# Kernel optimization log

Measured on AMD Instinct MI355X. Metric: run time of the kernel, lower is better.

Reference implementation:

```python
import jax, jax.numpy as jnp
import numpy as np
import math

N_HEAD = 16
N_EMBD = 2048
HEAD_DIM = 128
N_LAYER = 24
EPS = 1e-5


def _get_alibi_slopes(n_heads):
    def pow2(n):
        start = 2 ** (-2 ** (-(math.log2(n) - 3)))
        return [start * start ** i for i in range(n)]
    if math.log2(n_heads).is_integer():
        return pow2(n_heads)
    c = 2 ** math.floor(math.log2(n_heads))
    s = pow2(c)
    extra = _get_alibi_slopes(2 * c)
    return s + extra[0::2][: n_heads - c]

ALIBI_SLOPES = jnp.asarray(np.array(_get_alibi_slopes(N_HEAD), dtype=np.float32))  # (H,)


def rmsnorm(x, w, eps=EPS):
    # fp32 RMSNorm over last dim with affine weight (use_fp32=True path)
    xf = x.astype(jnp.float32)
    out = xf * jax.lax.rsqrt(jnp.mean(xf * xf, axis=-1, keepdims=True) + eps)
    return (out * w.astype(jnp.float32)).astype(x.dtype)


def setup_inputs() -> dict:
    key = jax.random.key(0)
    ks = jax.random.split(key, 8)
    B, T, C, H, D = 2, 2048, N_EMBD, N_HEAD, HEAD_DIM
    sc = 1.0 / math.sqrt(C)
    proj_std = 0.5 / math.sqrt(C) / math.sqrt(N_LAYER)
    return {
        "x": jax.random.normal(ks[0], (B, T, C), jnp.float32),
        "Wq": jax.random.normal(ks[1], (C, H * D), jnp.float32) * sc,
        "Wk": jax.random.normal(ks[2], (C, H * D), jnp.float32) * sc,
        "Wv": jax.random.normal(ks[3], (C, H * D), jnp.float32) * sc,
        "Wproj": jax.random.normal(ks[4], (H * D, C), jnp.float32) * proj_std,
        "q_rms_w": jnp.ones((D,), jnp.float32),
        "k_rms_w": jnp.ones((D,), jnp.float32),
        "subln_w": jnp.ones((D,), jnp.float32),
    }


def reference(x, Wq, Wk, Wv, Wproj, q_rms_w, k_rms_w, subln_w):
    B, T, C = x.shape
    H, D = N_HEAD, HEAD_DIM
    q = (x @ Wq).reshape(B, T, H, D)
    k = (x @ Wk).reshape(B, T, H, D)
    v = (x @ Wv).reshape(B, T, H, D)
    # QK RMSNorm over head_dim
    q = rmsnorm(q, q_rms_w)
    k = rmsnorm(k, k_rms_w)
    # ALiBi bias: -slope * max(i-j, 0), plus causal mask
    idx = jnp.arange(T)
    dist = jnp.maximum(idx[:, None] - idx[None, :], 0).astype(jnp.float32)  # (T,T)
    bias = -dist[None, :, :] * ALIBI_SLOPES[:, None, None]  # (H,T,T)
    causal = idx[:, None] >= idx[None, :]  # (T,T)
    scale = 1.0 / math.sqrt(D)
    scores = jnp.einsum("bthd,bshd->bhts", q, k) * scale + bias[None]  # (B,H,T,T)
    scores = jnp.where(causal[None, None], scores, -jnp.inf)
    attn = jax.nn.softmax(scores, axis=-1)
    y = jnp.einsum("bhts,bshd->bhtd", attn, v)  # (B,H,T,D)
    y = rmsnorm(y, subln_w)  # post-attention groupnorm (subln)
    y = y.transpose(0, 2, 1, 3).reshape(B, T, H * D)
    return y @ Wproj
```

## Files before the change

### kernel.cpp

```cpp
#include <hip/hip_runtime.h>
#include <hip/hip_bf16.h>

#define Bc 2
#define Tc 2048
#define Cc 2048
#define Hc 16
#define Dc 128
#define BTc 4096
#define NQ 6144
#define EPSc 1e-5f
#define QSCALE 0.08838834764831845f

typedef __attribute__((ext_vector_type(8))) short bf16x8;
typedef __attribute__((ext_vector_type(4))) short bf16x4;
typedef __attribute__((ext_vector_type(4))) float f32x4;

typedef struct { unsigned short u[4]; } us4;

__device__ __forceinline__ f32x4 mfma16(bf16x8 a, bf16x8 b, f32x4 c) {
  return __builtin_amdgcn_mfma_f32_16x16x32_bf16(a, b, c, 0, 0, 0);
}

__device__ __forceinline__ void gload16(const void* g, void* l) {
  __builtin_amdgcn_global_load_lds(
      (const __attribute__((address_space(1))) void*)g,
      (__attribute__((address_space(3))) void*)l, 16, 0, 0);
}

__global__ __launch_bounds__(256) void k_xconv(const float* __restrict__ x,
                                               __hip_bfloat16* __restrict__ xb) {
  size_t i = ((size_t)blockIdx.x * 256 + threadIdx.x) * 4;
  float4 v = *(const float4*)(x + i);
  union { __hip_bfloat16 h[4]; bf16x4 v4; } u;
  u.h[0] = __float2bfloat16(v.x); u.h[1] = __float2bfloat16(v.y);
  u.h[2] = __float2bfloat16(v.z); u.h[3] = __float2bfloat16(v.w);
  *(bf16x4*)(xb + i) = u.v4;
}

__global__ __launch_bounds__(256) void k_wconv(const float* __restrict__ Wq,
    const float* __restrict__ Wk, const float* __restrict__ Wv,
    const float* __restrict__ Wp, __hip_bfloat16* __restrict__ Wqkv_t,
    __hip_bfloat16* __restrict__ Wproj_t) {
  __shared__ float tile[64][65];
  int z = blockIdx.z;
  const float* src = (z == 0) ? Wq : (z == 1) ? Wk : (z == 2) ? Wv : Wp;
  __hip_bfloat16* dst = (z < 3) ? (Wqkv_t + (size_t)z * Cc * Cc) : Wproj_t;
  int k0 = blockIdx.x * 64, n0 = blockIdx.y * 64;
  int c = threadIdx.x & 63, rb = threadIdx.x >> 6;
  for (int i = 0; i < 16; i++) {
    int r = rb * 16 + i;
    tile[r][c] = src[(size_t)(k0 + r) * Cc + n0 + c];
  }
  __syncthreads();
  for (int i = 0; i < 16; i++) {
    int r = rb * 16 + i;
    dst[(size_t)(n0 + r) * Cc + k0 + c] = __float2bfloat16(tile[c][r]);
  }
}

__device__ __forceinline__ void mm48(f32x4 (&acc)[4][8], const bf16x8 (&A_)[4],
                                     const bf16x8 (&B_)[8]) {
  __builtin_amdgcn_s_setprio(1);
#pragma unroll
  for (int m = 0; m < 4; m++)
#pragma unroll
    for (int n = 0; n < 8; n++)
      acc[m][n] = mfma16(A_[m], B_[n], acc[m][n]);
  __builtin_amdgcn_s_setprio(0);
}

template <int MODE, typename OutT>
__global__ __launch_bounds__(256, 2) void k_gemm4(const __hip_bfloat16* __restrict__ A,
    const __hip_bfloat16* __restrict__ Bt, OutT* __restrict__ Co,
    int M, int N, const float* __restrict__ qw, const float* __restrict__ kw,
    __hip_bfloat16* __restrict__ Vt) {
  constexpr int K = 2048;
  __shared__ __align__(16) char lds[73728];
  const int nbx = M >> 7;
  const int nwg = nbx * (N >> 8);
  const int wg = blockIdx.x;
  const int swz = (wg & 7) * (nwg >> 3) + (wg >> 3);
  const int bx = swz % nbx, by = swz / nbx;
  const int tid = threadIdx.x, lane = tid & 63, wid = tid >> 6;
  const int wr = wid >> 1, wc = wid & 1;
  const int lr = lane & 15, lg = lane >> 4;
  const int xs = lg ^ ((lr >> 1) & 3);
  const int aoffR = (wr * 64 + lr) * 64 + xs * 16;
  const int boffR = 8192 + (wc * 128 + lr) * 64 + xs * 16;
  const int srow = lane >> 2;
  const int scolE = (((lane & 3) ^ ((lane >> 3) & 3)) << 3);
  const __hip_bfloat16* Ag = A + (size_t)(bx * 128 + wid * 32 + srow) * K + scolE;
  const __hip_bfloat16* Bg = Bt + (size_t)(by * 256 + wid * 64 + srow) * K + scolE;
  const size_t rK16 = (size_t)16 * K;
  char* dA = lds + wid * 2048;
  char* dB = lds + 8192 + wid * 4096;

#define STG(BUF, TS) {                                                   \
    gload16(Ag + (TS) * 32,        dA + (BUF) * 24576);                  \
    gload16(Ag + rK16 + (TS) * 32, dA + (BUF) * 24576 + 1024);           \
    gload16(Bg + (TS) * 32,            dB + (BUF) * 24576);              \
    gload16(Bg + rK16 + (TS) * 32,     dB + (BUF) * 24576 + 1024);       \
    gload16(Bg + 2 * rK16 + (TS) * 32, dB + (BUF) * 24576 + 2048);       \
    gload16(Bg + 3 * rK16 + (TS) * 32, dB + (BUF) * 24576 + 3072);       \
  }
#define BARRIER asm volatile("s_barrier" ::: "memory")
#define VW6 asm volatile("s_waitcnt vmcnt(6)" ::: "memory")
#define VW0 asm volatile("s_waitcnt vmcnt(0)" ::: "memory")

  f32x4 acc[4][8];
#pragma unroll
  for (int m = 0; m < 4; m++)
#pragma unroll
    for (int n = 0; n < 8; n++) acc[m][n] = f32x4{0.f, 0.f, 0.f, 0.f};
  bf16x8 rA[4], rB[8];

#define PH(RB, SB, TS, DOSTG, ENDW) {                                    \
    _Pragma("unroll")                                                    \
    for (int m = 0; m < 4; m++)                                          \
      rA[m] = *(const bf16x8*)(lds + (RB) * 24576 + aoffR + m * 1024);   \
    _Pragma("unroll")                                                    \
    for (int n = 0; n < 8; n++)                                          \
      rB[n] = *(const bf16x8*)(lds + (RB) * 24576 + boffR + n * 1024);   \
    if (DOSTG) STG((SB), (TS));                                          \
    mm48(acc, rA, rB);                                                   \
    ENDW;                                                                \
    BARRIER;                                                             \
  }

  STG(0, 0); STG(1, 1);
  VW6;
  BARRIER;

  for (int i = 0; i < 20; ++i) {
    const int t = 3 * i;
    PH(0, 2, t + 2, 1, VW6);
    PH(1, 0, t + 3, 1, VW6);
    PH(2, 1, t + 4, 1, VW6);
  }
  PH(0, 2, 62, 1, VW6);
  PH(1, 0, 63, 1, VW6);
  PH(2, 0, 0, 0, VW0);
  PH(0, 0, 0, 0, (void)0);
#undef PH
#undef STG
#undef BARRIER
#undef VW6
#undef VW0

  const int row0 = bx * 128 + wr * 64 + lg * 4;
  const int col0 = by * 256 + wc * 128 + lr;

  if (MODE == 1) {
    const int region = by >> 3;
    if (region < 2) {
      const float* wsel = (region == 0) ? qw : kw;
      const float extra = (region == 0) ? QSCALE : 1.0f;
      float wv[8];
#pragma unroll
      for (int n = 0; n < 8; n++) wv[n] = wsel[n * 16 + lr];
#pragma unroll
      for (int m = 0; m < 4; m++) {
        float ss[4] = {0.f, 0.f, 0.f, 0.f};
#pragma unroll
        for (int n = 0; n < 8; n++)
#pragma unroll
          for (int r = 0; r < 4; r++) ss[r] += acc[m][n][r] * acc[m][n][r];
        for (int msk = 1; msk < 16; msk <<= 1)
#pragma unroll
          for (int r = 0; r < 4; r++) ss[r] += __shfl_xor(ss[r], msk);
        float sc[4];
#pragma unroll
        for (int r = 0; r < 4; r++)
          sc[r] = rsqrtf(ss[r] * (1.0f / Dc) + EPSc) * extra;
#pragma unroll
        for (int n = 0; n < 8; n++) {
          size_t base = (size_t)(row0 + m * 16) * N + col0 + n * 16;
#pragma unroll
          for (int r = 0; r < 4; r++)
            ((__hip_bfloat16*)Co)[base + (size_t)r * N] =
                __float2bfloat16(acc[m][n][r] * sc[r] * wv[n]);
        }
      }
    } else {
      const int h = ((by - 16) * 256 + wc * 128) >> 7;
      const int bat = bx >> 4;
#pragma unroll
      for (int m = 0; m < 4; m++) {
        const int t0 = (row0 + m * 16) & (Tc - 1);
#pragma unroll
        for (int n = 0; n < 8; n++) {
          union { us4 p; unsigned long long q; } u;
#pragma unroll
          for (int r = 0; r < 4; r++) {
            union { __hip_bfloat16 h16; unsigned short s; } cv;
            cv.h16 = __float2bfloat16(acc[m][n][r]);
            u.p.u[r] = cv.s;
          }
          __hip_bfloat16* dst = Vt +
              ((size_t)(bat * 16 + h) * 128 + n * 16 + lr) * Tc + t0;
          *(unsigned long long*)dst = u.q;
        }
      }
    }
  } else {
#pragma unroll
    for (int m = 0; m < 4; m++)
#pragma unroll
      for (int n = 0; n < 8; n++) {
        size_t base = (size_t)(row0 + m * 16) * N + col0 + n * 16;
#pragma unroll
        for (int r = 0; r < 4; r++) {
          float v = acc[m][n][r];
          if constexpr (sizeof(OutT) == 2)
            Co[base + (size_t)r * N] = __float2bfloat16(v);
          else
            Co[base + (size_t)r * N] = v;
        }
      }
  }
}

__global__ __launch_bounds__(256, 2) void k_attn(const __hip_bfloat16* __restrict__ QKV,
    const __hip_bfloat16* __restrict__ Vt, const float* __restrict__ subw,
    __hip_bfloat16* __restrict__ Y) {
  __shared__ __align__(16) __hip_bfloat16 Ks[2][64][128];
  __shared__ __align__(16) __hip_bfloat16 Vs[2][128][64];
  __shared__ __align__(16) __hip_bfloat16 Plds[4][16][72];
  const int bh = blockIdx.x, pp = blockIdx.y;
  const int b = bh >> 4, h = bh & 15;
  const int w = threadIdx.x >> 6, lane = threadIdx.x & 63;
  const int lr = lane & 15, lg = lane >> 4;
  const float slope = exp2f(-0.5f * (float)(h + 1));
  const __hip_bfloat16* Kbase = QKV + (size_t)b * Tc * NQ + Cc + h * Dc;
  const __hip_bfloat16* Vbase = Vt + (size_t)bh * Dc * Tc;
  const int krow = (lane >> 4);
  const int kcolb = ((lane & 15) << 4);
  const int vrow = (lane >> 3);
  const int vcolb = ((lane & 7) << 4);
  f32x4 zero = {0.f, 0.f, 0.f, 0.f};

#define STAGE(bb, t)                                                              \
    {                                                                             \
      const int s0_ = (t) * 64;                                                   \
      for (int j = 0; j < 4; j++) {                                               \
        int row = w * 16 + j * 4 + krow;                                          \
        int cb = kcolb ^ ((row & 7) << 4);                                        \
        gload16(Kbase + (size_t)(s0_ + row) * NQ + (cb >> 1),                     \
                &Ks[bb][w * 16 + j * 4][0]);                                      \
      }                                                                           \
      for (int j = 0; j < 4; j++) {                                               \
        int row = w * 32 + j * 8 + vrow;                                          \
        int cb = vcolb ^ ((row & 7) << 4);                                        \
        gload16(Vbase + (size_t)row * Tc + s0_ + (cb >> 1),                       \
                &Vs[bb][w * 32 + j * 8][0]);                                      \
      }                                                                           \
    }
#define SBAR asm volatile("s_barrier" ::: "memory")
#define AVW8 asm volatile("s_waitcnt vmcnt(8)" ::: "memory")
#define AVW0 asm volatile("s_waitcnt vmcnt(0)" ::: "memory")
#define ALG0 asm volatile("s_waitcnt lgkmcnt(0)" ::: "memory")

  int buf = 0;
  for (int ti = 0; ti < 2; ti++) {
    const int qt = (ti == 0) ? (31 - pp) : pp;
    const int q0 = qt * 64 + w * 16;
    const int nchunk = qt + 1;
    bf16x8 aq[4];
    {
      const __hip_bfloat16* qb = QKV + (size_t)(b * Tc + q0 + lr) * NQ + h * Dc + lg * 8;
      for (int c = 0; c < 4; c++) aq[c] = *(const bf16x8*)(qb + c * 32);
    }
    f32x4 acc[8];
    for (int d = 0; d < 8; d++) acc[d] = zero;
    float mrow[4] = {-1e30f, -1e30f, -1e30f, -1e30f};
    float lrow[4] = {0.f, 0.f, 0.f, 0.f};

    SBAR;
    STAGE(buf, 0);
    for (int t = 0; t < nchunk; t++) {
      if (t + 1 < nchunk) { STAGE(buf ^ 1, t + 1); AVW8; }
      else                { AVW0; }
      SBAR;
      const int s0 = t * 64;
      f32x4 s[4];
      for (int ss = 0; ss < 4; ss++) s[ss] = zero;
      __builtin_amdgcn_s_setprio(1);
      for (int c = 0; c < 4; c++)
        for (int ss = 0; ss < 4; ss++) {
          int kr = ss * 16 + lr;
          const bf16x8 kf = *(const bf16x8*)
              &Ks[buf][kr][((c * 64 + lg * 16) ^ ((kr & 7) << 4)) >> 1];
          s[ss] = mfma16(aq[c], kf, s[ss]);
        }
      __builtin_amdgcn_s_setprio(0);
      float ps[4][4], mt[4];
      for (int r = 0; r < 4; r++) mt[r] = -1e30f;
      for (int ss = 0; ss < 4; ss++) {
        int jj = s0 + ss * 16 + lr;
        for (int r = 0; r < 4; r++) {
          int i = q0 + lg * 4 + r;
          float pv = (jj <= i) ? s[ss][r] - slope * (float)(i - jj) : -1e30f;
          ps[ss][r] = pv;
          mt[r] = fmaxf(mt[r], pv);
        }
      }
      for (int m = 1; m < 16; m <<= 1)
        for (int r = 0; r < 4; r++) mt[r] = fmaxf(mt[r], __shfl_xor(mt[r], m));
      float corr[4], rs[4];
      for (int r = 0; r < 4; r++) {
        float mn = fmaxf(mrow[r], mt[r]);
        corr[r] = __expf(mrow[r] - mn);
        mrow[r] = mn;
        rs[r] = 0.f;
      }
      for (int ss = 0; ss < 4; ss++)
        for (int r = 0; r < 4; r++) {
          float e = __expf(ps[ss][r] - mrow[r]);
          ps[ss][r] = e;
          rs[r] += e;
        }
      for (int m = 1; m < 16; m <<= 1)
        for (int r = 0; r < 4; r++) rs[r] += __shfl_xor(rs[r], m);
      for (int r = 0; r < 4; r++) lrow[r] = lrow[r] * corr[r] + rs[r];
      for (int d = 0; d < 8; d++)
        for (int r = 0; r < 4; r++) acc[d][r] *= corr[r];
      for (int ss = 0; ss < 4; ss++)
        for (int r = 0; r < 4; r++)
          Plds[w][lg * 4 + r][ss * 16 + lr] = __float2bfloat16(ps[ss][r]);
      bf16x8 pa0 = *(const bf16x8*)&Plds[w][lr][lg * 8];
      bf16x8 pa1 = *(const bf16x8*)&Plds[w][lr][32 + lg * 8];
      __builtin_amdgcn_s_setprio(1);
      for (int d = 0; d < 8; d++) {
        int vr = d * 16 + lr;
        const bf16x8 b0 = *(const bf16x8*)
            &Vs[buf][vr][((lg * 16) ^ ((vr & 7) << 4)) >> 1];
        const bf16x8 b1 = *(const bf16x8*)
            &Vs[buf][vr][((64 + lg * 16) ^ ((vr & 7) << 4)) >> 1];
        acc[d] = mfma16(pa0, b0, acc[d]);
        acc[d] = mfma16(pa1, b1, acc[d]);
      }
      __builtin_amdgcn_s_setprio(0);
      ALG0; SBAR;
      buf ^= 1;
    }
    float ssum[4] = {0.f, 0.f, 0.f, 0.f};
    for (int r = 0; r < 4; r++) {
      float rl = 1.0f / lrow[r];
      for (int d = 0; d < 8; d++) {
        float o = acc[d][r] * rl;
        acc[d][r] = o;
        ssum[r] += o * o;
      }
    }
    for (int m = 1; m < 16; m <<= 1)
      for (int r = 0; r < 4; r++) ssum[r] += __shfl_xor(ssum[r], m);
    float ms[4];
    for (int r = 0; r < 4; r++) ms[r] = rsqrtf(ssum[r] * (1.0f / Dc) + EPSc);
    for (int d = 0; d < 8; d++) {
      float wv = subw[d * 16 + lr];
      for (int r = 0; r < 4; r++) {
        float y = acc[d][r] * ms[r] * wv;
        Y[(size_t)(b * Tc + q0 + lg * 4 + r) * Cc + h * Dc + d * 16 + lr] =
            __float2bfloat16(y);
      }
    }
  }
#undef STAGE
#undef SBAR
#undef AVW8
#undef AVW0
#undef ALG0
}

extern "C" void kernel_launch(void* const* d_in, const int* in_sizes, int n_in,
                              void* d_out, int out_size, void* d_ws, size_t ws_size,
                              hipStream_t stream) {
  const float* x  = (const float*)d_in[0];
  const float* Wq = (const float*)d_in[1];
  const float* Wk = (const float*)d_in[2];
  const float* Wv = (const float*)d_in[3];
  const float* Wp = (const float*)d_in[4];
  const float* qw = (const float*)d_in[5];
  const float* kw = (const float*)d_in[6];
  const float* sw = (const float*)d_in[7];
  float* out = (float*)d_out;

  char* ws = (char*)d_ws;
  __hip_bfloat16* Xb    = (__hip_bfloat16*)(ws + 0);
  __hip_bfloat16* Wqkv  = (__hip_bfloat16*)(ws + 16777216);
  __hip_bfloat16* Wproj = (__hip_bfloat16*)(ws + 41943040);
  __hip_bfloat16* QKV   = (__hip_bfloat16*)(ws + 50331648);
  __hip_bfloat16* Vt    = (__hip_bfloat16*)(ws + 100663296);
  __hip_bfloat16* Yb    = (__hip_bfloat16*)(ws + 117440512);

  k_xconv<<<dim3((BTc * Cc) / 1024), 256, 0, stream>>>(x, Xb);
  k_wconv<<<dim3(32, 32, 4), 256, 0, stream>>>(Wq, Wk, Wv, Wp, Wqkv, Wproj);
  k_gemm4<1, __hip_bfloat16><<<dim3((BTc / 128) * (NQ / 256)), 256, 0, stream>>>(
      Xb, Wqkv, QKV, BTc, NQ, qw, kw, Vt);
  k_attn<<<dim3(Bc * Hc, 16), 256, 0, stream>>>(QKV, Vt, sw, Yb);
  k_gemm4<0, float><<<dim3((BTc / 128) * (Cc / 256)), 256, 0, stream>>>(
      Yb, Wproj, out, BTc, Cc, nullptr, nullptr, nullptr);
}
```

Before: 262.0 us.

## Load GEMM A operand directly to registers, stage only B in LDS

The A tile is no longer staged through LDS. Each wave now loads its own A fragments straight from global memory into double-buffered registers, one K-step ahead, while B keeps the triple-buffered LDS path. This cuts LDS footprint from 72KB to 48KB and removes the LDS write/read traffic for A. In exchange it adds register pressure and uncoalesced 16-byte global loads whose latency is hidden only one phase ahead, and waves sharing the same rows fetch duplicate A data.

```diff
diff --git a/kernel.cpp b/kernel.cpp
--- a/kernel.cpp
+++ b/kernel.cpp
@@ -70,12 +70,12 @@
 }
 
 template <int MODE, typename OutT>
-__global__ __launch_bounds__(256, 2) void k_gemm4(const __hip_bfloat16* __restrict__ A,
+__global__ __launch_bounds__(256, 2) void k_gemm4r(const __hip_bfloat16* __restrict__ A,
     const __hip_bfloat16* __restrict__ Bt, OutT* __restrict__ Co,
     int M, int N, const float* __restrict__ qw, const float* __restrict__ kw,
     __hip_bfloat16* __restrict__ Vt) {
   constexpr int K = 2048;
-  __shared__ __align__(16) char lds[73728];
+  __shared__ __align__(16) char lds[49152];
   const int nbx = M >> 7;
   const int nwg = nbx * (N >> 8);
   const int wg = blockIdx.x;
@@ -85,67 +85,68 @@
   const int wr = wid >> 1, wc = wid & 1;
   const int lr = lane & 15, lg = lane >> 4;
   const int xs = lg ^ ((lr >> 1) & 3);
-  const int aoffR = (wr * 64 + lr) * 64 + xs * 16;
-  const int boffR = 8192 + (wc * 128 + lr) * 64 + xs * 16;
+  const int boffR = (wc * 128 + lr) * 64 + xs * 16;
   const int srow = lane >> 2;
   const int scolE = (((lane & 3) ^ ((lane >> 3) & 3)) << 3);
-  const __hip_bfloat16* Ag = A + (size_t)(bx * 128 + wid * 32 + srow) * K + scolE;
   const __hip_bfloat16* Bg = Bt + (size_t)(by * 256 + wid * 64 + srow) * K + scolE;
   const size_t rK16 = (size_t)16 * K;
-  char* dA = lds + wid * 2048;
-  char* dB = lds + 8192 + wid * 4096;
-
-#define STG(BUF, TS) {                                                   \
-    gload16(Ag + (TS) * 32,        dA + (BUF) * 24576);                  \
-    gload16(Ag + rK16 + (TS) * 32, dA + (BUF) * 24576 + 1024);           \
-    gload16(Bg + (TS) * 32,            dB + (BUF) * 24576);              \
-    gload16(Bg + rK16 + (TS) * 32,     dB + (BUF) * 24576 + 1024);       \
-    gload16(Bg + 2 * rK16 + (TS) * 32, dB + (BUF) * 24576 + 2048);       \
-    gload16(Bg + 3 * rK16 + (TS) * 32, dB + (BUF) * 24576 + 3072);       \
-  }
+  char* dB = lds + wid * 4096;
+  const __hip_bfloat16* Agl = A + (size_t)(bx * 128 + wr * 64 + lr) * K + lg * 8;
+
+#define STGB(BUF, TS) { const __hip_bfloat16* g_ = Bg + (TS) * 32;        \
+    gload16(g_,            dB + (BUF) * 16384);                           \
+    gload16(g_ + rK16,     dB + (BUF) * 16384 + 1024);                    \
+    gload16(g_ + 2 * rK16, dB + (BUF) * 16384 + 2048);                    \
+    gload16(g_ + 3 * rK16, dB + (BUF) * 16384 + 3072); }
+#define LDA(REG, T) { _Pragma("unroll")                                   \
+    for (int m = 0; m < 4; m++)                                           \
+      REG[m] = *(const bf16x8*)(Agl + m * rK16 + (size_t)(T) * 32); }
 #define BARRIER asm volatile("s_barrier" ::: "memory")
-#define VW6 asm volatile("s_waitcnt vmcnt(6)" ::: "memory")
-#define VW0 asm volatile("s_waitcnt vmcnt(0)" ::: "memory")
+#define VW8 asm volatile("s_waitcnt vmcnt(8)" ::: "memory")
+#define VW4 asm volatile("s_waitcnt vmcnt(4)" ::: "memory")
 
   f32x4 acc[4][8];
 #pragma unroll
   for (int m = 0; m < 4; m++)
 #pragma unroll
     for (int n = 0; n < 8; n++) acc[m][n] = f32x4{0.f, 0.f, 0.f, 0.f};
-  bf16x8 rA[4], rB[8];
-
-#define PH(RB, SB, TS, DOSTG, ENDW) {                                    \
-    _Pragma("unroll")                                                    \
-    for (int m = 0; m < 4; m++)                                          \
-      rA[m] = *(const bf16x8*)(lds + (RB) * 24576 + aoffR + m * 1024);   \
-    _Pragma("unroll")                                                    \
-    for (int n = 0; n < 8; n++)                                          \
-      rB[n] = *(const bf16x8*)(lds + (RB) * 24576 + boffR + n * 1024);   \
-    if (DOSTG) STG((SB), (TS));                                          \
-    mm48(acc, rA, rB);                                                   \
-    ENDW;                                                                \
-    BARRIER;                                                             \
-  }
-
-  STG(0, 0); STG(1, 1);
-  VW6;
+  bf16x8 rA0[4], rA1[4], rB[8];
+
+#define PH(RB, SB, TS, AC, AN, TA, DOA, DOSTG, ENDW) {                    \
+    _Pragma("unroll")                                                     \
+    for (int n = 0; n < 8; n++)                                           \
+      rB[n] = *(const bf16x8*)(lds + (RB) * 16384 + boffR + n * 1024);    \
+    if (DOA) LDA(AN, TA);                                                 \
+    if (DOSTG) STGB((SB), (TS));                                          \
+    mm48(acc, AC, rB);                                                    \
+    ENDW;                                                                 \
+    BARRIER;                                                              \
+  }
+
+  STGB(0, 0); STGB(1, 1);
+  LDA(rA0, 0);
+  VW8;
   BARRIER;
 
-  for (int i = 0; i < 20; ++i) {
-    const int t = 3 * i;
-    PH(0, 2, t + 2, 1, VW6);
-    PH(1, 0, t + 3, 1, VW6);
-    PH(2, 1, t + 4, 1, VW6);
-  }
-  PH(0, 2, 62, 1, VW6);
-  PH(1, 0, 63, 1, VW6);
-  PH(2, 0, 0, 0, VW0);
-  PH(0, 0, 0, 0, (void)0);
+  for (int i = 0; i < 10; ++i) {
+    const int t = 6 * i;
+    PH(0, 2, t + 2, rA0, rA1, t + 1, 1, 1, VW8);
+    PH(1, 0, t + 3, rA1, rA0, t + 2, 1, 1, VW8);
+    PH(2, 1, t + 4, rA0, rA1, t + 3, 1, 1, VW8);
+    PH(0, 2, t + 5, rA1, rA0, t + 4, 1, 1, VW8);
+    PH(1, 0, t + 6, rA0, rA1, t + 5, 1, 1, VW8);
+    PH(2, 1, t + 7, rA1, rA0, t + 6, 1, 1, VW8);
+  }
+  PH(0, 2, 62, rA0, rA1, 61, 1, 1, VW8);
+  PH(1, 0, 63, rA1, rA0, 62, 1, 1, VW8);
+  PH(2, 0, 0,  rA0, rA1, 63, 1, 0, VW4);
+  PH(0, 0, 0,  rA1, rA0, 0,  0, 0, (void)0);
 #undef PH
-#undef STG
+#undef STGB
+#undef LDA
 #undef BARRIER
-#undef VW6
-#undef VW0
+#undef VW8
+#undef VW4
 
   const int row0 = bx * 128 + wr * 64 + lg * 4;
   const int col0 = by * 256 + wc * 128 + lr;
@@ -395,9 +396,9 @@
 
   k_xconv<<<dim3((BTc * Cc) / 1024), 256, 0, stream>>>(x, Xb);
   k_wconv<<<dim3(32, 32, 4), 256, 0, stream>>>(Wq, Wk, Wv, Wp, Wqkv, Wproj);
-  k_gemm4<1, __hip_bfloat16><<<dim3((BTc / 128) * (NQ / 256)), 256, 0, stream>>>(
+  k_gemm4r<1, __hip_bfloat16><<<dim3((BTc / 128) * (NQ / 256)), 256, 0, stream>>>(
       Xb, Wqkv, QKV, BTc, NQ, qw, kw, Vt);
   k_attn<<<dim3(Bc * Hc, 16), 256, 0, stream>>>(QKV, Vt, sw, Yb);
-  k_gemm4<0, float><<<dim3((BTc / 128) * (Cc / 256)), 256, 0, stream>>>(
+  k_gemm4r<0, float><<<dim3((BTc / 128) * (Cc / 256)), 256, 0, stream>>>(
       Yb, Wproj, out, BTc, Cc, nullptr, nullptr, nullptr);
 }
```

Result: slower. 341.0 us (+30.2%).
